# Performance work log

Measured on AMD Instinct MI355X. Metric: run time of the kernel, lower is better.

The kernel has to match this reference:

```python
import jax, jax.numpy as jnp
import numpy as np

B, S, E = 2, 2048, 4096
H, KVH, D = 32, 8, 128          # query heads, kv heads, head_dim
GROUPS = H // KVH               # 4
WINDOW = 4096                   # sliding window (>= S -> fully causal)
ROPE_THETA = 10000.0


def _rope_sin_cos(position_ids):
    # inv_freq over even dims, freqs duplicated (Mixtral/GPT-NeoX style)
    inv_freq = 1.0 / (ROPE_THETA ** (jnp.arange(0, D, 2, dtype=jnp.float32) / D))  # [D/2]
    freqs = position_ids.astype(jnp.float32)[..., None] * inv_freq  # [B,S,D/2]
    emb = jnp.concatenate((freqs, freqs), axis=-1)                  # [B,S,D]
    # add head axis for broadcasting against [B,S,H,D]
    return jnp.sin(emb)[:, :, None, :], jnp.cos(emb)[:, :, None, :]


def _rotate_half(x):
    return jnp.concatenate((-x[..., D // 2:], x[..., :D // 2]), axis=-1)


def setup_inputs() -> dict:
    key = jax.random.key(0)
    ks = jax.random.split(key, 5)
    w_scale = 1.0 / np.sqrt(E)
    hidden_states = jax.random.normal(ks[0], (B, S, E), jnp.float32)
    Wq = jax.random.normal(ks[1], (E, H * D), jnp.float32) * w_scale
    Wk = jax.random.normal(ks[2], (E, KVH * D), jnp.float32) * w_scale
    Wv = jax.random.normal(ks[3], (E, KVH * D), jnp.float32) * w_scale
    Wo = jax.random.normal(ks[4], (H * D, E), jnp.float32) * w_scale
    # sliding-window causal mask: tril then zero entries more than WINDOW back
    causal = jnp.tril(jnp.ones((S, S), dtype=bool))
    causal = jnp.triu(causal, k=-WINDOW)[None, None]  # [1,1,S,S]
    attention_mask = jnp.ones((B, S), jnp.int32)
    position_ids = jnp.broadcast_to(jnp.arange(S, dtype=jnp.int32), (B, S))
    return dict(hidden_states=hidden_states, Wq=Wq, Wk=Wk, Wv=Wv, Wo=Wo,
                causal_mask=causal, attention_mask=attention_mask,
                position_ids=position_ids)


def reference(hidden_states, Wq, Wk, Wv, Wo, causal_mask, attention_mask, position_ids):
    # projections + head split
    q = (hidden_states @ Wq).reshape(B, S, H, D)
    k = (hidden_states @ Wk).reshape(B, S, KVH, D)
    v = (hidden_states @ Wv).reshape(B, S, KVH, D)

    # inline RoPE on q and k
    sin, cos = _rope_sin_cos(position_ids)
    q = q * cos + _rotate_half(q) * sin
    k = k * cos + _rotate_half(k) * sin

    # GQA: repeat kv heads to match query heads
    k = jnp.repeat(k, GROUPS, axis=2)  # [B,S,H,D]
    v = jnp.repeat(v, GROUPS, axis=2)

    # combined mask -> additive bias
    mask = causal_mask[:, :, :S, :S] & (attention_mask[:, None, None, :] > 0)  # [B|1,1,S,S]
    bias = jnp.where(mask, 0.0, jnp.finfo(jnp.float32).min)

    scores = jnp.einsum('bqhd,bkhd->bhqk', q, k) / jnp.sqrt(jnp.float32(D)) + bias
    probs = jax.nn.softmax(scores, axis=-1)
    attn = jnp.einsum('bhqk,bkhd->bqhd', probs, v).reshape(B, S, H * D)
    return attn @ Wo
```

## Files before the change

kernel.cpp:

```cpp
#include <hip/hip_runtime.h>
#include <hip/hip_bf16.h>
#include <cstdint>
#include <cstddef>

#define B_ 2
#define S_ 2048
#define E_ 4096
#define H_ 32
#define KVH_ 8
#define D_ 128
#define M_ (B_*S_)
#define HD_ (H_*D_)
#define KVD_ (KVH_*D_)
#define NQKV_ 6144

typedef unsigned short u16;
typedef __attribute__((ext_vector_type(8))) short bf16x8;
typedef __attribute__((ext_vector_type(4))) float f32x4;

__device__ __forceinline__ float bf2f(u16 u) {
  union { float f; uint32_t i; } v; v.i = ((uint32_t)u) << 16; return v.f;
}
__device__ __forceinline__ u16 f2bf(float f) {
  union { float f; uint32_t i; } v; v.f = f;
  uint32_t r = v.i + 0x7FFF + ((v.i >> 16) & 1);
  return (u16)(r >> 16);
}

__device__ __forceinline__ void gload_lds16(const void* g, void* l) {
  __builtin_amdgcn_global_load_lds(
      (const __attribute__((address_space(1))) void*)g,
      (__attribute__((address_space(3))) void*)l, 16, 0, 0);
}

#define FENCE() asm volatile("" ::: "memory")
#define BARRIER() do { FENCE(); __builtin_amdgcn_s_barrier(); FENCE(); } while (0)
#define VMCNT6() asm volatile("s_waitcnt vmcnt(6)" ::: "memory")
#define VMCNT2() asm volatile("s_waitcnt vmcnt(2)" ::: "memory")

__global__ __launch_bounds__(256) void k_f2bf(const float* __restrict__ in,
                                              u16* __restrict__ out, int n) {
  int i = (blockIdx.x * 256 + threadIdx.x) * 4;
  if (i + 3 < n) {
    float4 v = *(const float4*)(in + i);
    *(ushort4*)(out + i) = make_ushort4(f2bf(v.x), f2bf(v.y), f2bf(v.z), f2bf(v.w));
  }
}

__global__ __launch_bounds__(256) void k_transpose_f2bf(const float* __restrict__ in,
                                                        u16* __restrict__ out, int R, int C) {
  __shared__ float tile[64][65];
  const int c0 = blockIdx.x * 64, r0 = blockIdx.y * 64;
  const int tid = threadIdx.x;
  const int lx = tid & 63, ty = tid >> 6;
#pragma unroll
  for (int i = 0; i < 16; ++i)
    tile[ty + 4 * i][lx] = in[(size_t)(r0 + ty + 4 * i) * C + c0 + lx];
  __syncthreads();
  const int oy = tid & 31, xb = tid >> 5;
#pragma unroll
  for (int i = 0; i < 8; ++i) {
    int X = xb + 8 * i;
    *(ushort2*)(out + (size_t)(c0 + X) * R + r0 + 2 * oy) =
        make_ushort2(f2bf(tile[2 * oy][X]), f2bf(tile[2 * oy + 1][X]));
  }
}

__global__ __launch_bounds__(256) void k_transpose_v(const u16* __restrict__ vlin,
                                                     u16* __restrict__ vt, int stride) {
  __shared__ u16 tile[64][65];
  const int bk = blockIdx.z;
  const int b = bk >> 3, kvh = bk & 7;
  const int s0 = blockIdx.x * 64, d0 = blockIdx.y * 64;
  const int tid = threadIdx.x;
  const int lx = tid & 63, ty = tid >> 6;
#pragma unroll
  for (int i = 0; i < 16; ++i)
    tile[ty + 4 * i][lx] =
        vlin[(size_t)(b * S_ + s0 + ty + 4 * i) * stride + kvh * D_ + d0 + lx];
  __syncthreads();
  const int oy = tid & 31, xb = tid >> 5;
#pragma unroll
  for (int i = 0; i < 8; ++i) {
    int X = xb + 8 * i;
    *(ushort2*)(vt + ((size_t)bk * D_ + d0 + X) * S_ + s0 + 2 * oy) =
        make_ushort2(tile[2 * oy][X], tile[2 * oy + 1][X]);
  }
}

__global__ __launch_bounds__(256) void k_table(float2* __restrict__ tab) {
  int i = blockIdx.x * 256 + threadIdx.x;
  if (i < S_ * 64) {
    int s = i >> 6, d = i & 63;
    float inv = powf(10000.0f, -(float)d / 64.0f);
    float f = (float)s * inv;
    tab[i] = make_float2(sinf(f), cosf(f));
  }
}

__global__ __launch_bounds__(256) void k_rope(const u16* __restrict__ in, u16* __restrict__ out,
                                              const float2* __restrict__ tab,
                                              const int* __restrict__ pos,
                                              int heads, int in_stride, int total) {
  int i = blockIdx.x * 256 + threadIdx.x;
  if (i >= total) return;
  int d = i & 63;
  int s = (i >> 6) & (S_ - 1);
  int bh = i >> 17;
  int h = bh % heads, b = bh / heads;
  size_t ibase = ((size_t)(b * S_ + s)) * in_stride + h * D_;
  float2 scv = tab[pos[b * S_ + s] * 64 + d];
  float x1 = bf2f(in[ibase + d]), x2 = bf2f(in[ibase + d + 64]);
  size_t obase = ((size_t)bh * S_ + s) * D_;
  out[obase + d]      = f2bf(x1 * scv.y - x2 * scv.x);
  out[obase + d + 64] = f2bf(x2 * scv.y + x1 * scv.x);
}

template<bool OUTF32>
__global__ __launch_bounds__(512, 2) void k_gemm8(const u16* __restrict__ A,
                                                  const u16* __restrict__ BT,
                                                  void* __restrict__ Cp,
                                                  int M, int N, int K) {
  __shared__ __align__(16) u16 L[8 * 8192];
  const int tid = threadIdx.x;
  const int w = tid >> 6, lane = tid & 63;
  const int lrow = lane & 15, lk = lane >> 4;
  const int nbn = N >> 8;
  const int tm = blockIdx.x / nbn, tn = blockIdx.x % nbn;
  const int m0 = tm << 8, n0 = tn << 8;
  const int wm = w >> 2, wn = w & 3;

  f32x4 acc[8][4] = {};
  bf16x8 bres[4][2];
  const int nt = K >> 6;

  const u16* RA[2] = { &L[(0 + wm) * 8192],       &L[(4 + wm) * 8192] };
  const u16* RB[2] = { &L[(2 + (wn >> 1)) * 8192], &L[(6 + (wn >> 1)) * 8192] };

  auto STAGE = [&](int buf, int mat, int half, int t) {
    const u16* src = mat ? BT : A;
    const int base0 = mat ? n0 : m0;
    u16* reg = &L[(buf * 4 + mat * 2 + half) * 8192];
#pragma unroll
    for (int c = 0; c < 2; ++c) {
      int rl = (c << 6) + (w << 3) + (lane >> 3);
      int gb = (lane & 7) ^ (rl & 7);
      gload_lds16(src + (size_t)(base0 + (half << 7) + rl) * K + (t << 6) + (gb << 3),
                  reg + ((c << 6) + (w << 3)) * 64);
    }
  };
  auto LDB = [&](int buf) {
#pragma unroll
    for (int nf = 0; nf < 4; ++nf)
#pragma unroll
      for (int ks = 0; ks < 2; ++ks) {
        int br = ((wn & 1) << 6) + (nf << 4) + lrow;
        int cb = (ks << 2) + lk;
        bres[nf][ks] = *(const bf16x8*)(RB[buf] + br * 64 + ((cb ^ (br & 7)) << 3));
      }
  };
  auto LDA2 = [&](int buf, int mp, bf16x8 (&af)[2][2]) {
#pragma unroll
    for (int d = 0; d < 2; ++d)
#pragma unroll
      for (int ks = 0; ks < 2; ++ks) {
        int ar = (((mp << 1) + d) << 4) + lrow;
        int cb = (ks << 2) + lk;
        af[d][ks] = *(const bf16x8*)(RA[buf] + ar * 64 + ((cb ^ (ar & 7)) << 3));
      }
  };
  auto MM2 = [&](int mp, bf16x8 (&af)[2][2]) {
    __builtin_amdgcn_s_setprio(1);
#pragma unroll
    for (int ks = 0; ks < 2; ++ks)
#pragma unroll
      for (int d = 0; d < 2; ++d)
#pragma unroll
        for (int nf = 0; nf < 4; ++nf)
          acc[(mp << 1) + d][nf] = __builtin_amdgcn_mfma_f32_16x16x32_bf16(
              af[d][ks], bres[nf][ks], acc[(mp << 1) + d][nf], 0, 0, 0);
    __builtin_amdgcn_s_setprio(0);
  };

  STAGE(0, 1, 0, 0); STAGE(0, 1, 1, 0);
  STAGE(0, 0, 0, 0); STAGE(0, 0, 1, 0);
  STAGE(1, 1, 0, 1); STAGE(1, 1, 1, 1);

  const int niter = nt >> 1;
  for (int i = 0; i < niter; ++i) {
    const int t1 = 2 * i + 1;
    const int t2 = (2 * i + 2 < nt) ? 2 * i + 2 : nt - 1;
    const int t3 = (2 * i + 3 < nt) ? 2 * i + 3 : nt - 1;
    bf16x8 afA[2][2], afB[2][2];

    STAGE(1, 0, 0, t1);
    VMCNT6();
    BARRIER();
    LDB(0); LDA2(0, 0, afA);
    MM2(0, afA);
    LDA2(0, 1, afB);
    BARRIER();
    STAGE(1, 0, 1, t1);
    MM2(1, afB);
    LDA2(0, 2, afA);
    BARRIER();
    STAGE(0, 1, 0, t2);
    MM2(2, afA);
    LDA2(0, 3, afB);
    BARRIER();
    STAGE(0, 1, 1, t2);
    MM2(3, afB);
    BARRIER();

    STAGE(0, 0, 0, t2);
    VMCNT6();
    BARRIER();
    LDB(1); LDA2(1, 0, afA);
    MM2(0, afA);
    LDA2(1, 1, afB);
    BARRIER();
    STAGE(0, 0, 1, t2);
    MM2(1, afB);
    LDA2(1, 2, afA);
    BARRIER();
    STAGE(1, 1, 0, t3);
    MM2(2, afA);
    LDA2(1, 3, afB);
    BARRIER();
    STAGE(1, 1, 1, t3);
    MM2(3, afB);
    BARRIER();
  }

#pragma unroll
  for (int mi = 0; mi < 8; ++mi)
#pragma unroll
    for (int nf = 0; nf < 4; ++nf) {
      int col = n0 + (wn << 6) + (nf << 4) + lrow;
#pragma unroll
      for (int j = 0; j < 4; ++j) {
        int row = m0 + (wm << 7) + (mi << 4) + (lk << 2) + j;
        if (OUTF32) ((float*)Cp)[(size_t)row * N + col] = acc[mi][nf][j];
        else        ((u16*)Cp)[(size_t)row * N + col]  = f2bf(acc[mi][nf][j]);
      }
    }
}

__global__ __launch_bounds__(512, 2) void k_gemm8n(const u16* __restrict__ A,
                                                   const u16* __restrict__ BT,
                                                   u16* __restrict__ Cp,
                                                   int M, int N, int K) {
  __shared__ __align__(16) u16 LA[2 * 4 * 4096];
  __shared__ __align__(16) u16 LB[2 * 3 * 4096];
  const int tid = threadIdx.x;
  const int w = tid >> 6, lane = tid & 63;
  const int lrow = lane & 15, lk = lane >> 4;
  const int nbn = N / 192;
  const int tm = blockIdx.x / nbn, tn = blockIdx.x % nbn;
  const int m0 = tm << 8, n0 = tn * 192;
  const int wm = w >> 2, wn = w & 3;

  f32x4 acc[8][3] = {};
  bf16x8 bres[3][2];
  const int nt = K >> 6;

  const int srow = (w << 3) + (lane >> 3);
  const int sgb = (lane & 7) ^ (srow & 7);

  auto SA = [&](int buf, int u, int t) {
    gload_lds16(A + (size_t)(m0 + (u << 6) + srow) * K + (t << 6) + (sgb << 3),
                &LA[((buf << 2) + u) * 4096 + (w << 9)]);
  };
  auto SB = [&](int buf, int u, int t) {
    gload_lds16(BT + (size_t)(n0 + (u << 6) + srow) * K + (t << 6) + (sgb << 3),
                &LB[(buf * 3 + u) * 4096 + (w << 9)]);
  };
  auto LDB = [&](int buf) {
#pragma unroll
    for (int nf = 0; nf < 3; ++nf)
#pragma unroll
      for (int ks = 0; ks < 2; ++ks) {
        int br = wn * 48 + (nf << 4) + lrow;
        int cb = (ks << 2) + lk;
        bres[nf][ks] = *(const bf16x8*)(&LB[(buf * 3 + (br >> 6)) * 4096]
                                        + (br & 63) * 64 + ((cb ^ (br & 7)) << 3));
      }
  };
  auto LDA2 = [&](int buf, int mp, bf16x8 (&af)[2][2]) {
#pragma unroll
    for (int d = 0; d < 2; ++d)
#pragma unroll
      for (int ks = 0; ks < 2; ++ks) {
        int ar = (wm << 7) + (mp << 5) + (d << 4) + lrow;
        int cb = (ks << 2) + lk;
        af[d][ks] = *(const bf16x8*)(&LA[((buf << 2) + (ar >> 6)) * 4096]
                                     + (ar & 63) * 64 + ((cb ^ (ar & 7)) << 3));
      }
  };
  auto MM2 = [&](int mp, bf16x8 (&af)[2][2]) {
    __builtin_amdgcn_s_setprio(1);
#pragma unroll
    for (int ks = 0; ks < 2; ++ks)
#pragma unroll
      for (int d = 0; d < 2; ++d)
#pragma unroll
        for (int nf = 0; nf < 3; ++nf)
          acc[(mp << 1) + d][nf] = __builtin_amdgcn_mfma_f32_16x16x32_bf16(
              af[d][ks], bres[nf][ks], acc[(mp << 1) + d][nf], 0, 0, 0);
    __builtin_amdgcn_s_setprio(0);
  };

  SB(0, 0, 0); SB(0, 1, 0); SB(0, 2, 0);
  SA(0, 0, 0); SA(0, 1, 0); SA(0, 2, 0); SA(0, 3, 0);

  const int niter = nt >> 1;
  for (int i = 0; i < niter; ++i) {
    const int t1 = 2 * i + 1;
    const int t2 = (2 * i + 2 < nt) ? 2 * i + 2 : nt - 1;
    bf16x8 afA[2][2], afB[2][2];

    SB(1, 0, t1); SB(1, 1, t1);
    VMCNT2();
    BARRIER();
    LDB(0); LDA2(0, 0, afA);
    MM2(0, afA);
    LDA2(0, 1, afB);
    BARRIER();
    SB(1, 2, t1); SA(1, 0, t1);
    MM2(1, afB);
    LDA2(0, 2, afA);
    BARRIER();
    SA(1, 1, t1); SA(1, 2, t1);
    MM2(2, afA);
    LDA2(0, 3, afB);
    BARRIER();
    SA(1, 3, t1);
    MM2(3, afB);
    BARRIER();

    SB(0, 0, t2); SB(0, 1, t2);
    VMCNT2();
    BARRIER();
    LDB(1); LDA2(1, 0, afA);
    MM2(0, afA);
    LDA2(1, 1, afB);
    BARRIER();
    SB(0, 2, t2); SA(0, 0, t2);
    MM2(1, afB);
    LDA2(1, 2, afA);
    BARRIER();
    SA(0, 1, t2); SA(0, 2, t2);
    MM2(2, afA);
    LDA2(1, 3, afB);
    BARRIER();
    SA(0, 3, t2);
    MM2(3, afB);
    BARRIER();
  }

#pragma unroll
  for (int mi = 0; mi < 8; ++mi)
#pragma unroll
    for (int nf = 0; nf < 3; ++nf) {
      int col = n0 + wn * 48 + (nf << 4) + lrow;
#pragma unroll
      for (int j = 0; j < 4; ++j) {
        int row = m0 + (wm << 7) + (mi << 4) + (lk << 2) + j;
        Cp[(size_t)row * N + col] = f2bf(acc[mi][nf][j]);
      }
    }
}

__global__ __launch_bounds__(512, 4) void k_attn(const u16* __restrict__ QKV,
                                                 const u16* __restrict__ Kr,
                                                 const u16* __restrict__ Vt,
                                                 const float2* __restrict__ tab,
                                                 const int* __restrict__ pos,
                                                 u16* __restrict__ ctx) {
  __shared__ __align__(16) u16 Ks[2][64 * 128];
  __shared__ __align__(16) u16 Vs[2][144 * 64];
  __shared__ __align__(16) u16 Ps[8][16 * 40];
  const int bid = blockIdx.x;
  const int qt = 15 - (bid >> 6);
  const int bh = bid & 63;
  const int b = bh >> 5, h = bh & 31;
  const int kvh = h >> 2;
  const int tid = threadIdx.x;
  const int w = tid >> 6, lane = tid & 63;
  const int lrow = lane & 15, lk = lane >> 4;
  const int q0w = qt * 128 + w * 16;

  const float cl = 0.12751743435f;
  const int s = q0w + lrow;
  const int p = pos[b * S_ + s];
  const u16* q0 = QKV + ((size_t)(b * S_ + s)) * NQKV_ + h * D_ + lk * 8;
  bf16x8 raw[4];
#pragma unroll
  for (int ks = 0; ks < 4; ++ks) raw[ks] = *(const bf16x8*)(q0 + ks * 32);
  bf16x8 qf[4];
#pragma unroll
  for (int ks = 0; ks < 2; ++ks)
#pragma unroll
    for (int e = 0; e < 8; ++e) {
      int d = ks * 32 + lk * 8 + e;
      float2 scv = tab[p * 64 + d];
      float x1 = bf2f((u16)raw[ks][e]), x2 = bf2f((u16)raw[ks + 2][e]);
      qf[ks][e]     = (short)f2bf(cl * (x1 * scv.y - x2 * scv.x));
      qf[ks + 2][e] = (short)f2bf(cl * (x2 * scv.y + x1 * scv.x));
    }

  float m[4] = {-1e30f, -1e30f, -1e30f, -1e30f};
  f32x4 o[9] = {};

  const u16* kbase = Kr + (size_t)(b * KVH_ + kvh) * S_ * D_;
  const u16* vbase = Vt + (size_t)(b * KVH_ + kvh) * D_ * S_;
  const int nt = 2 * qt + 2;

  auto STAGE = [&](int buf, int kb) {
    const int kv0 = kb << 6;
#pragma unroll
    for (int c = 0; c < 2; ++c) {
      int r = w * 8 + (lane >> 4) + c * 4;
      gload_lds16(kbase + (size_t)(kv0 + r) * D_ + (((lane & 15) ^ (r & 7)) << 3),
                  &Ks[buf][(w * 8 + c * 4) * 128]);
    }
#pragma unroll
    for (int c = 0; c < 2; ++c) {
      int r = w * 16 + (lane >> 3) + c * 8;
      gload_lds16(vbase + (size_t)r * S_ + kv0 + (((lane & 7) ^ (r & 7)) << 3),
                  &Vs[buf][(w * 16 + c * 8) * 64]);
    }
  };

  for (int i = tid; i < 16 * 64; i += 512) {
    u16 v = (i < 64) ? (u16)0x3F80 : (u16)0;
    Vs[0][128 * 64 + i] = v;
    Vs[1][128 * 64 + i] = v;
  }
  asm volatile("s_waitcnt lgkmcnt(0)" ::: "memory");

  STAGE(0, 0);
  int cur = 0;
  for (int kb = 0; kb < nt; ++kb) {
    if (kb + 1 < nt) {
      STAGE(cur ^ 1, kb + 1);
      asm volatile("s_waitcnt vmcnt(4)" ::: "memory");
    } else {
      asm volatile("s_waitcnt vmcnt(0)" ::: "memory");
    }
    BARRIER();
    const int kv0 = kb << 6;
    if (kv0 <= q0w + 15) {
      const u16* Kb = &Ks[cur][0];
      const u16* Vb = &Vs[cur][0];

      f32x4 sc[4] = {};
      __builtin_amdgcn_s_setprio(1);
#pragma unroll
      for (int n0 = 0; n0 < 4; ++n0) {
#pragma unroll
        for (int ks = 0; ks < 4; ++ks) {
          int krow = (n0 << 4) + lrow;
          bf16x8 kf = *(const bf16x8*)(Kb + krow * 128 + ((((ks << 2) + lk) ^ (krow & 7)) << 3));
          sc[n0] = __builtin_amdgcn_mfma_f32_16x16x32_bf16(qf[ks], kf, sc[n0], 0, 0, 0);
        }
      }
      __builtin_amdgcn_s_setprio(0);

      const bool diag = (kv0 + 63 > q0w);
      float mnew[4] = {m[0], m[1], m[2], m[3]};
#pragma unroll
      for (int n0 = 0; n0 < 4; ++n0)
#pragma unroll
        for (int j = 0; j < 4; ++j) {
          float v = sc[n0][j];
          if (diag && (kv0 + (n0 << 4) + lrow > q0w + (lk << 2) + j)) v = -1e30f;
          sc[n0][j] = v;
          mnew[j] = fmaxf(mnew[j], v);
        }
#pragma unroll
      for (int j = 0; j < 4; ++j) {
        float v = mnew[j];
        v = fmaxf(v, __shfl_xor(v, 1));
        v = fmaxf(v, __shfl_xor(v, 2));
        v = fmaxf(v, __shfl_xor(v, 4));
        v = fmaxf(v, __shfl_xor(v, 8));
        mnew[j] = v;
      }

      bool need = false;
#pragma unroll
      for (int j = 0; j < 4; ++j) need |= (mnew[j] - m[j] > 11.5f);
      if (__any(need)) {
        float alpha[4];
#pragma unroll
        for (int j = 0; j < 4; ++j) {
          alpha[j] = exp2f(m[j] - mnew[j]);
          m[j] = mnew[j];
        }
#pragma unroll
        for (int db = 0; db < 9; ++db)
#pragma unroll
          for (int j = 0; j < 4; ++j)
            o[db][j] *= alpha[j];
      }

#pragma unroll
      for (int n0 = 0; n0 < 4; ++n0)
#pragma unroll
        for (int j = 0; j < 4; ++j)
          sc[n0][j] = exp2f(sc[n0][j] - m[j]);

      u16* pw = &Ps[w][0];
#pragma unroll
      for (int half = 0; half < 2; ++half) {
        asm volatile("s_waitcnt lgkmcnt(0)" ::: "memory");
#pragma unroll
        for (int n0 = 0; n0 < 2; ++n0)
#pragma unroll
          for (int j = 0; j < 4; ++j)
            pw[((lk << 2) + j) * 40 + (n0 << 4) + lrow] =
                f2bf(sc[(half << 1) + n0][j]);
        bf16x8 pf = *(const bf16x8*)(pw + lrow * 40 + (lk << 3));
        __builtin_amdgcn_s_setprio(1);
#pragma unroll
        for (int db = 0; db < 9; ++db) {
          int dr = (db << 4) + lrow;
          bf16x8 vf = *(const bf16x8*)(Vb + dr * 64 + ((((half << 2) + lk) ^ (dr & 7)) << 3));
          o[db] = __builtin_amdgcn_mfma_f32_16x16x32_bf16(pf, vf, o[db], 0, 0, 0);
        }
        __builtin_amdgcn_s_setprio(0);
      }
    }
    BARRIER();
    cur ^= 1;
  }

  float linv[4];
#pragma unroll
  for (int j = 0; j < 4; ++j) linv[j] = 1.0f / __shfl(o[8][j], lane & 48);
#pragma unroll
  for (int db = 0; db < 8; ++db)
#pragma unroll
    for (int j = 0; j < 4; ++j) {
      int q = q0w + (lk << 2) + j;
      ctx[((size_t)(b * S_ + q)) * HD_ + h * D_ + (db << 4) + lrow] = f2bf(o[db][j] * linv[j]);
    }
}

extern "C" void kernel_launch(void* const* d_in, const int* in_sizes, int n_in,
                              void* d_out, int out_size, void* d_ws, size_t ws_size,
                              hipStream_t stream) {
  const float* hidden = (const float*)d_in[0];
  const float* Wq = (const float*)d_in[1];
  const float* Wk = (const float*)d_in[2];
  const float* Wv = (const float*)d_in[3];
  const float* Wo = (const float*)d_in[4];
  const int* pos_ids = (const int*)d_in[7];

  char* ws = (char*)d_ws;
  u16* hs      = (u16*)(ws);
  u16* ctx     = hs;
  u16* wqkvt   = (u16*)(ws + 33554432ull);
  u16* wot     = wqkvt;
  u16* qkvlin  = (u16*)(ws + 83886080ull);
  u16* kr      = (u16*)(ws + 134217728ull);
  u16* vt      = (u16*)(ws + 142606336ull);
  float2* tab  = (float2*)(ws + 150994944ull);

  k_f2bf<<<dim3((M_*E_)/1024), dim3(256), 0, stream>>>(hidden, hs, M_*E_);
  k_transpose_f2bf<<<dim3(HD_/64, E_/64), dim3(256), 0, stream>>>(Wq, wqkvt, E_, HD_);
  k_transpose_f2bf<<<dim3(KVD_/64, E_/64), dim3(256), 0, stream>>>(Wk, wqkvt + (size_t)HD_*E_, E_, KVD_);
  k_transpose_f2bf<<<dim3(KVD_/64, E_/64), dim3(256), 0, stream>>>(Wv, wqkvt + (size_t)(HD_+KVD_)*E_, E_, KVD_);
  k_gemm8n<<<dim3((M_/256)*(NQKV_/192)), dim3(512), 0, stream>>>(hs, wqkvt, qkvlin, M_, NQKV_, E_);
  k_transpose_f2bf<<<dim3(E_/64, HD_/64), dim3(256), 0, stream>>>(Wo, wot, HD_, E_);
  k_table<<<dim3((S_*64)/256), dim3(256), 0, stream>>>(tab);
  k_rope<<<dim3((B_*KVH_*S_*64)/256), dim3(256), 0, stream>>>(qkvlin + HD_, kr, tab, pos_ids, KVH_, NQKV_, B_*KVH_*S_*64);
  k_transpose_v<<<dim3(S_/64, D_/64, B_*KVH_), dim3(256), 0, stream>>>(qkvlin + HD_ + KVD_, vt, NQKV_);
  k_attn<<<dim3(B_*H_*(S_/128)), dim3(512), 0, stream>>>(qkvlin, kr, vt, tab, pos_ids, ctx);
  k_gemm8<true><<<dim3((M_/256)*(E_/256)), dim3(512), 0, stream>>>(ctx, wot, d_out, M_, E_, HD_);
}
```

Measured before the change: 585.1 us.

## Split-K the fused QKV projection GEMM and sum partials in consumers

The QKV projection GEMM switches from 256x192 tiles to the 256x256 tile kernel layout and, when the workspace is large enough, splits K into two halves over a second grid dimension that write separate bf16 partial outputs. The rope, V-transpose and attention kernels then add the two partials when reading. This doubles the block count for a GEMM that had only 512 blocks, to improve CU occupancy and tail behavior. In exchange it writes an extra partial buffer, adds extra reads and bf16 rounding in the consumers, and depends on ws_size at runtime.

Result: faster. 565.9 us (-3.3%).

```diff
diff --git a/kernel.cpp b/kernel.cpp
--- a/kernel.cpp
+++ b/kernel.cpp
@@ -36,7 +36,6 @@
 #define FENCE() asm volatile("" ::: "memory")
 #define BARRIER() do { FENCE(); __builtin_amdgcn_s_barrier(); FENCE(); } while (0)
 #define VMCNT6() asm volatile("s_waitcnt vmcnt(6)" ::: "memory")
-#define VMCNT2() asm volatile("s_waitcnt vmcnt(2)" ::: "memory")
 
 __global__ __launch_bounds__(256) void k_f2bf(const float* __restrict__ in,
                                               u16* __restrict__ out, int n) {
@@ -67,6 +66,8 @@
 }
 
 __global__ __launch_bounds__(256) void k_transpose_v(const u16* __restrict__ vlin,
+                                                     const u16* __restrict__ vlin2,
+                                                     int two,
                                                      u16* __restrict__ vt, int stride) {
   __shared__ u16 tile[64][65];
   const int bk = blockIdx.z;
@@ -75,9 +76,11 @@
   const int tid = threadIdx.x;
   const int lx = tid & 63, ty = tid >> 6;
 #pragma unroll
-  for (int i = 0; i < 16; ++i)
-    tile[ty + 4 * i][lx] =
-        vlin[(size_t)(b * S_ + s0 + ty + 4 * i) * stride + kvh * D_ + d0 + lx];
+  for (int i = 0; i < 16; ++i) {
+    size_t idx = (size_t)(b * S_ + s0 + ty + 4 * i) * stride + kvh * D_ + d0 + lx;
+    u16 a = vlin[idx];
+    tile[ty + 4 * i][lx] = two ? f2bf(bf2f(a) + bf2f(vlin2[idx])) : a;
+  }
   __syncthreads();
   const int oy = tid & 31, xb = tid >> 5;
 #pragma unroll
@@ -98,7 +101,9 @@
   }
 }
 
-__global__ __launch_bounds__(256) void k_rope(const u16* __restrict__ in, u16* __restrict__ out,
+__global__ __launch_bounds__(256) void k_rope(const u16* __restrict__ in,
+                                              const u16* __restrict__ in2, int two,
+                                              u16* __restrict__ out,
                                               const float2* __restrict__ tab,
                                               const int* __restrict__ pos,
                                               int heads, int in_stride, int total) {
@@ -111,6 +116,7 @@
   size_t ibase = ((size_t)(b * S_ + s)) * in_stride + h * D_;
   float2 scv = tab[pos[b * S_ + s] * 64 + d];
   float x1 = bf2f(in[ibase + d]), x2 = bf2f(in[ibase + d + 64]);
+  if (two) { x1 += bf2f(in2[ibase + d]); x2 += bf2f(in2[ibase + d + 64]); }
   size_t obase = ((size_t)bh * S_ + s) * D_;
   out[obase + d]      = f2bf(x1 * scv.y - x2 * scv.x);
   out[obase + d + 64] = f2bf(x2 * scv.y + x1 * scv.x);
@@ -246,44 +252,49 @@
     }
 }
 
-__global__ __launch_bounds__(512, 2) void k_gemm8n(const u16* __restrict__ A,
+__global__ __launch_bounds__(512, 2) void k_gemm8s(const u16* __restrict__ A,
                                                    const u16* __restrict__ BT,
-                                                   u16* __restrict__ Cp,
-                                                   int M, int N, int K) {
-  __shared__ __align__(16) u16 LA[2 * 4 * 4096];
-  __shared__ __align__(16) u16 LB[2 * 3 * 4096];
+                                                   u16* __restrict__ out0,
+                                                   u16* __restrict__ out1,
+                                                   int M, int N, int lda, int klen) {
+  __shared__ __align__(16) u16 L[8 * 8192];
   const int tid = threadIdx.x;
   const int w = tid >> 6, lane = tid & 63;
   const int lrow = lane & 15, lk = lane >> 4;
-  const int nbn = N / 192;
+  const int nbn = N >> 8;
   const int tm = blockIdx.x / nbn, tn = blockIdx.x % nbn;
-  const int m0 = tm << 8, n0 = tn * 192;
+  const int m0 = tm << 8, n0 = tn << 8;
   const int wm = w >> 2, wn = w & 3;
-
-  f32x4 acc[8][3] = {};
-  bf16x8 bres[3][2];
-  const int nt = K >> 6;
-
-  const int srow = (w << 3) + (lane >> 3);
-  const int sgb = (lane & 7) ^ (srow & 7);
-
-  auto SA = [&](int buf, int u, int t) {
-    gload_lds16(A + (size_t)(m0 + (u << 6) + srow) * K + (t << 6) + (sgb << 3),
-                &LA[((buf << 2) + u) * 4096 + (w << 9)]);
-  };
-  auto SB = [&](int buf, int u, int t) {
-    gload_lds16(BT + (size_t)(n0 + (u << 6) + srow) * K + (t << 6) + (sgb << 3),
-                &LB[(buf * 3 + u) * 4096 + (w << 9)]);
+  const int kofs = blockIdx.y * klen;
+  u16* Cp = blockIdx.y ? out1 : out0;
+
+  f32x4 acc[8][4] = {};
+  bf16x8 bres[4][2];
+  const int nt = klen >> 6;
+
+  const u16* RA[2] = { &L[(0 + wm) * 8192],       &L[(4 + wm) * 8192] };
+  const u16* RB[2] = { &L[(2 + (wn >> 1)) * 8192], &L[(6 + (wn >> 1)) * 8192] };
+
+  auto STAGE = [&](int buf, int mat, int half, int t) {
+    const u16* src = mat ? BT : A;
+    const int base0 = mat ? n0 : m0;
+    u16* reg = &L[(buf * 4 + mat * 2 + half) * 8192];
+#pragma unroll
+    for (int c = 0; c < 2; ++c) {
+      int rl = (c << 6) + (w << 3) + (lane >> 3);
+      int gb = (lane & 7) ^ (rl & 7);
+      gload_lds16(src + (size_t)(base0 + (half << 7) + rl) * lda + kofs + (t << 6) + (gb << 3),
+                  reg + ((c << 6) + (w << 3)) * 64);
+    }
   };
   auto LDB = [&](int buf) {
 #pragma unroll
-    for (int nf = 0; nf < 3; ++nf)
+    for (int nf = 0; nf < 4; ++nf)
 #pragma unroll
       for (int ks = 0; ks < 2; ++ks) {
-        int br = wn * 48 + (nf << 4) + lrow;
+        int br = ((wn & 1) << 6) + (nf << 4) + lrow;
         int cb = (ks << 2) + lk;
-        bres[nf][ks] = *(const bf16x8*)(&LB[(buf * 3 + (br >> 6)) * 4096]
-                                        + (br & 63) * 64 + ((cb ^ (br & 7)) << 3));
+        bres[nf][ks] = *(const bf16x8*)(RB[buf] + br * 64 + ((cb ^ (br & 7)) << 3));
       }
   };
   auto LDA2 = [&](int buf, int mp, bf16x8 (&af)[2][2]) {
@@ -291,10 +302,9 @@
     for (int d = 0; d < 2; ++d)
 #pragma unroll
       for (int ks = 0; ks < 2; ++ks) {
-        int ar = (wm << 7) + (mp << 5) + (d << 4) + lrow;
+        int ar = (((mp << 1) + d) << 4) + lrow;
         int cb = (ks << 2) + lk;
-        af[d][ks] = *(const bf16x8*)(&LA[((buf << 2) + (ar >> 6)) * 4096]
-                                     + (ar & 63) * 64 + ((cb ^ (ar & 7)) << 3));
+        af[d][ks] = *(const bf16x8*)(RA[buf] + ar * 64 + ((cb ^ (ar & 7)) << 3));
       }
   };
   auto MM2 = [&](int mp, bf16x8 (&af)[2][2]) {
@@ -304,56 +314,58 @@
 #pragma unroll
       for (int d = 0; d < 2; ++d)
 #pragma unroll
-        for (int nf = 0; nf < 3; ++nf)
+        for (int nf = 0; nf < 4; ++nf)
           acc[(mp << 1) + d][nf] = __builtin_amdgcn_mfma_f32_16x16x32_bf16(
               af[d][ks], bres[nf][ks], acc[(mp << 1) + d][nf], 0, 0, 0);
     __builtin_amdgcn_s_setprio(0);
   };
 
-  SB(0, 0, 0); SB(0, 1, 0); SB(0, 2, 0);
-  SA(0, 0, 0); SA(0, 1, 0); SA(0, 2, 0); SA(0, 3, 0);
+  STAGE(0, 1, 0, 0); STAGE(0, 1, 1, 0);
+  STAGE(0, 0, 0, 0); STAGE(0, 0, 1, 0);
+  STAGE(1, 1, 0, 1); STAGE(1, 1, 1, 1);
 
   const int niter = nt >> 1;
   for (int i = 0; i < niter; ++i) {
     const int t1 = 2 * i + 1;
     const int t2 = (2 * i + 2 < nt) ? 2 * i + 2 : nt - 1;
+    const int t3 = (2 * i + 3 < nt) ? 2 * i + 3 : nt - 1;
     bf16x8 afA[2][2], afB[2][2];
 
-    SB(1, 0, t1); SB(1, 1, t1);
-    VMCNT2();
+    STAGE(1, 0, 0, t1);
+    VMCNT6();
     BARRIER();
     LDB(0); LDA2(0, 0, afA);
     MM2(0, afA);
     LDA2(0, 1, afB);
     BARRIER();
-    SB(1, 2, t1); SA(1, 0, t1);
+    STAGE(1, 0, 1, t1);
     MM2(1, afB);
     LDA2(0, 2, afA);
     BARRIER();
-    SA(1, 1, t1); SA(1, 2, t1);
+    STAGE(0, 1, 0, t2);
     MM2(2, afA);
     LDA2(0, 3, afB);
     BARRIER();
-    SA(1, 3, t1);
+    STAGE(0, 1, 1, t2);
     MM2(3, afB);
     BARRIER();
 
-    SB(0, 0, t2); SB(0, 1, t2);
-    VMCNT2();
+    STAGE(0, 0, 0, t2);
+    VMCNT6();
     BARRIER();
     LDB(1); LDA2(1, 0, afA);
     MM2(0, afA);
     LDA2(1, 1, afB);
     BARRIER();
-    SB(0, 2, t2); SA(0, 0, t2);
+    STAGE(0, 0, 1, t2);
     MM2(1, afB);
     LDA2(1, 2, afA);
     BARRIER();
-    SA(0, 1, t2); SA(0, 2, t2);
+    STAGE(1, 1, 0, t3);
     MM2(2, afA);
     LDA2(1, 3, afB);
     BARRIER();
-    SA(0, 3, t2);
+    STAGE(1, 1, 1, t3);
     MM2(3, afB);
     BARRIER();
   }
@@ -361,8 +373,8 @@
 #pragma unroll
   for (int mi = 0; mi < 8; ++mi)
 #pragma unroll
-    for (int nf = 0; nf < 3; ++nf) {
-      int col = n0 + wn * 48 + (nf << 4) + lrow;
+    for (int nf = 0; nf < 4; ++nf) {
+      int col = n0 + (wn << 6) + (nf << 4) + lrow;
 #pragma unroll
       for (int j = 0; j < 4; ++j) {
         int row = m0 + (wm << 7) + (mi << 4) + (lk << 2) + j;
@@ -372,6 +384,7 @@
 }
 
 __global__ __launch_bounds__(512, 4) void k_attn(const u16* __restrict__ QKV,
+                                                 const u16* __restrict__ QKV2, int two,
                                                  const u16* __restrict__ Kr,
                                                  const u16* __restrict__ Vt,
                                                  const float2* __restrict__ tab,
@@ -393,10 +406,21 @@
   const float cl = 0.12751743435f;
   const int s = q0w + lrow;
   const int p = pos[b * S_ + s];
-  const u16* q0 = QKV + ((size_t)(b * S_ + s)) * NQKV_ + h * D_ + lk * 8;
+  const size_t qoff = ((size_t)(b * S_ + s)) * NQKV_ + h * D_ + lk * 8;
+  const u16* q0 = QKV + qoff;
   bf16x8 raw[4];
 #pragma unroll
   for (int ks = 0; ks < 4; ++ks) raw[ks] = *(const bf16x8*)(q0 + ks * 32);
+  if (two) {
+    const u16* q02 = QKV2 + qoff;
+#pragma unroll
+    for (int ks = 0; ks < 4; ++ks) {
+      bf16x8 r2 = *(const bf16x8*)(q02 + ks * 32);
+#pragma unroll
+      for (int e = 0; e < 8; ++e)
+        raw[ks][e] = (short)f2bf(bf2f((u16)raw[ks][e]) + bf2f((u16)r2[e]));
+    }
+  }
   bf16x8 qf[4];
 #pragma unroll
   for (int ks = 0; ks < 2; ++ks)
@@ -558,25 +582,34 @@
   const float* Wo = (const float*)d_in[4];
   const int* pos_ids = (const int*)d_in[7];
 
+  const size_t MiB = 1048576ull;
+  const bool split = ws_size >= 177 * MiB;
+  const int two = split ? 1 : 0;
+
   char* ws = (char*)d_ws;
   u16* hs      = (u16*)(ws);
   u16* ctx     = hs;
-  u16* wqkvt   = (u16*)(ws + 33554432ull);
+  u16* wqkvt   = (u16*)(ws + 32 * MiB);
   u16* wot     = wqkvt;
-  u16* qkvlin  = (u16*)(ws + 83886080ull);
-  u16* kr      = (u16*)(ws + 134217728ull);
-  u16* vt      = (u16*)(ws + 142606336ull);
-  float2* tab  = (float2*)(ws + 150994944ull);
+  u16* kr      = (u16*)(ws + 64 * MiB);
+  u16* vt      = (u16*)(ws + 72 * MiB);
+  u16* qkvlin  = (u16*)(ws + 80 * MiB);
+  u16* qkvlin2 = split ? (u16*)(ws + 128 * MiB) : qkvlin;
+  float2* tab  = (float2*)(ws + (split ? 176 : 128) * MiB);
 
   k_f2bf<<<dim3((M_*E_)/1024), dim3(256), 0, stream>>>(hidden, hs, M_*E_);
   k_transpose_f2bf<<<dim3(HD_/64, E_/64), dim3(256), 0, stream>>>(Wq, wqkvt, E_, HD_);
   k_transpose_f2bf<<<dim3(KVD_/64, E_/64), dim3(256), 0, stream>>>(Wk, wqkvt + (size_t)HD_*E_, E_, KVD_);
   k_transpose_f2bf<<<dim3(KVD_/64, E_/64), dim3(256), 0, stream>>>(Wv, wqkvt + (size_t)(HD_+KVD_)*E_, E_, KVD_);
-  k_gemm8n<<<dim3((M_/256)*(NQKV_/192)), dim3(512), 0, stream>>>(hs, wqkvt, qkvlin, M_, NQKV_, E_);
+  k_gemm8s<<<dim3((M_/256)*(NQKV_/256), split ? 2 : 1), dim3(512), 0, stream>>>(
+      hs, wqkvt, qkvlin, qkvlin2, M_, NQKV_, E_, split ? E_/2 : E_);
   k_transpose_f2bf<<<dim3(E_/64, HD_/64), dim3(256), 0, stream>>>(Wo, wot, HD_, E_);
   k_table<<<dim3((S_*64)/256), dim3(256), 0, stream>>>(tab);
-  k_rope<<<dim3((B_*KVH_*S_*64)/256), dim3(256), 0, stream>>>(qkvlin + HD_, kr, tab, pos_ids, KVH_, NQKV_, B_*KVH_*S_*64);
-  k_transpose_v<<<dim3(S_/64, D_/64, B_*KVH_), dim3(256), 0, stream>>>(qkvlin + HD_ + KVD_, vt, NQKV_);
-  k_attn<<<dim3(B_*H_*(S_/128)), dim3(512), 0, stream>>>(qkvlin, kr, vt, tab, pos_ids, ctx);
+  k_rope<<<dim3((B_*KVH_*S_*64)/256), dim3(256), 0, stream>>>(
+      qkvlin + HD_, qkvlin2 + HD_, two, kr, tab, pos_ids, KVH_, NQKV_, B_*KVH_*S_*64);
+  k_transpose_v<<<dim3(S_/64, D_/64, B_*KVH_), dim3(256), 0, stream>>>(
+      qkvlin + HD_ + KVD_, qkvlin2 + HD_ + KVD_, two, vt, NQKV_);
+  k_attn<<<dim3(B_*H_*(S_/128)), dim3(512), 0, stream>>>(
+      qkvlin, qkvlin2, two, kr, vt, tab, pos_ids, ctx);
   k_gemm8<true><<<dim3((M_/256)*(E_/256)), dim3(512), 0, stream>>>(ctx, wot, d_out, M_, E_, HD_);
 }
```
